# Kernel tuning notes

Hardware: AMD Instinct MI355X
Metric: run time of the kernel (lower is better)

## Reference

```python
import jax, jax.numpy as jnp
import numpy as np

BS, Z_DIM, HID, Z_IN, N_STEP, OUT_DIM = 4096, 512, 1024, 128, 32, 3


def setup_inputs() -> dict:
    key = jax.random.key(0)
    ks = jax.random.split(key, 12)
    s = 0.02
    return {
        "z": jax.random.normal(ks[0], (BS, Z_DIM), jnp.float32),
        "inference": 1,
        "tfr": 0,
        "W_zh": jax.random.normal(ks[1], (HID, Z_DIM), jnp.float32) * s,
        "b_zh": jnp.zeros((HID,), jnp.float32),
        "W_zi": jax.random.normal(ks[2], (Z_IN, Z_DIM), jnp.float32) * s,
        "b_zi": jnp.zeros((Z_IN,), jnp.float32),
        "W_ih": jax.random.normal(ks[3], (3 * HID, OUT_DIM + Z_IN), jnp.float32) * s,
        "b_ih": jnp.zeros((3 * HID,), jnp.float32),
        "W_hh": jax.random.normal(ks[4], (3 * HID, HID), jnp.float32) * s,
        "b_hh": jnp.zeros((3 * HID,), jnp.float32),
        "W_out": jax.random.normal(ks[5], (OUT_DIM, HID), jnp.float32) * s,
        "b_out": jnp.zeros((OUT_DIM,), jnp.float32),
        "init_input": jax.random.uniform(ks[6], (OUT_DIM,), jnp.float32),
    }


def reference(z, inference, tfr, W_zh, b_zh, W_zi, b_zi, W_ih, b_ih, W_hh, b_hh,
              W_out, b_out, init_input):
    bs = z.shape[0]
    h0 = z @ W_zh.T + b_zh                      # [B, H]   (z2dec_hid)
    z_in = z @ W_zi.T + b_zi                    # [B, Z_IN] (z2dec_in)
    token0 = jnp.broadcast_to(init_input, (bs, OUT_DIM))

    def step(carry, _):
        h, token = carry
        x = jnp.concatenate([token, z_in], axis=-1)     # [B, OUT_DIM+Z_IN]
        gi = x @ W_ih.T + b_ih                          # [B, 3H]
        gh = h @ W_hh.T + b_hh                          # [B, 3H]
        i_r, i_u, i_n = jnp.split(gi, 3, axis=-1)       # pytorch gate order r,z,n
        h_r, h_u, h_n = jnp.split(gh, 3, axis=-1)
        r = jax.nn.sigmoid(i_r + h_r)
        u = jax.nn.sigmoid(i_u + h_u)
        n = jnp.tanh(i_n + r * h_n)
        h_new = (1.0 - u) * n + u * h
        o = h_new @ W_out.T + b_out                     # [B, 3]
        bass = jax.nn.sigmoid(o[:, 0])
        rhy_int = o[:, 1]
        rhy = jax.nn.sigmoid(o[:, 2])
        out_feat = jnp.stack([bass, rhy_int, rhy], axis=-1)          # [B, 3]
        next_token = jnp.stack(
            [bass, rhy_int, (rhy > 0.5).astype(z.dtype)], axis=-1)  # [B, 3]
        return (h_new, next_token), out_feat

    _, outs = jax.lax.scan(step, (h0, token0), None, length=N_STEP)  # [T, B, 3]
    recon = jnp.transpose(outs, (1, 0, 2))                           # [B, T, 3]
    return recon
```

## Files before the change

kernel.cpp:

```cpp
#include <hip/hip_runtime.h>
#include <hip/hip_bf16.h>
#include <math.h>

#define BS   4096
#define ZD   512
#define HIDN 1024
#define ZINN 128
#define NST  32
#define NP   3072

typedef unsigned short u16;
typedef __bf16 bf16x8 __attribute__((ext_vector_type(8)));
typedef _Float16 f16x8 __attribute__((ext_vector_type(8)));
typedef float f32x4 __attribute__((ext_vector_type(4)));
typedef float f32x16 __attribute__((ext_vector_type(16)));

static __device__ __forceinline__ u16 bf_bits(float v) {
  __bf16 b = (__bf16)v;
  return __builtin_bit_cast(unsigned short, b);
}
static __device__ __forceinline__ float bf_val(float v) {
  return (float)(__bf16)v;
}
static __device__ __forceinline__ u16 h16_bits(float v) {
  _Float16 h = (_Float16)v;
  return __builtin_bit_cast(unsigned short, h);
}

static __device__ __forceinline__ void ld_lds16(const u16* g, u16* l) {
  __builtin_amdgcn_global_load_lds(
      (const __attribute__((address_space(1))) void*)g,
      (__attribute__((address_space(3))) void*)l, 16, 0, 0);
}

static __device__ __forceinline__ int r_orig(int w) {
  const int g = w / 96;
  const int rem = w - g * 96;
  const int j = rem >> 5, m = rem & 31;
  return j * 1024 + g * 32 + m;
}

static __device__ __forceinline__ size_t pk_off(int row, int col) {
  return ((size_t)(row >> 5) * 64 + (col >> 4)) * 512 +
         (((col >> 3) & 1) * 32 + (row & 31)) * 8 + (col & 7);
}
static __device__ __forceinline__ size_t pkz_off(int row, int col) {
  return ((size_t)(row >> 5) * 8 + (col >> 4)) * 512 +
         (((col >> 3) & 1) * 32 + (row & 31)) * 8 + (col & 7);
}


__global__ void k_split(const float* __restrict__ s, u16* __restrict__ hi,
                        u16* __restrict__ lo, int n) {
  int i = blockIdx.x * 256 + threadIdx.x;
  if (i >= n) return;
  float v = s[i];
  float h = bf_val(v);
  hi[i] = bf_bits(v);
  lo[i] = bf_bits(v - h);
}

__global__ void k_pack_whh(const float* __restrict__ W_hh, u16* __restrict__ Bpk) {
  int i = blockIdx.x * 256 + threadIdx.x;
  if (i >= NP * HIDN) return;
  const int w = i >> 10, k = i & 1023;
  const float v = W_hh[(size_t)r_orig(w) * HIDN + k];
  Bpk[pk_off(w, k)] = h16_bits(v);
}

__global__ void k_prep_wih(const float* __restrict__ W_ih, const float* __restrict__ b_ih,
                           const float* __restrict__ b_hh,
                           u16* __restrict__ Wpk,
                           float* __restrict__ wtok, float* __restrict__ cb0) {
  int i = blockIdx.x * 256 + threadIdx.x;
  if (i < NP * 128) {
    const int w = i >> 7, c = i & 127;
    const float v = W_ih[r_orig(w) * 131 + 3 + c];
    Wpk[pkz_off(w, c)] = h16_bits(v);
  }
  if (i < NP * 3) {
    const int w = i / 3, s = i - w * 3;
    wtok[i] = W_ih[r_orig(w) * 131 + s];
  }
  if (i < NP) {
    const int r = r_orig(i);
    cb0[i] = b_ih[r] + (r < 2048 ? b_hh[r] : 0.0f);
  }
}

__global__ void k_token_init(const float* __restrict__ init_input, float* __restrict__ token) {
  int i = blockIdx.x * 256 + threadIdx.x;
  if (i < BS * 4) token[i] = ((i & 3) < 3) ? init_input[i & 3] : 0.0f;
}

template <int OUTMODE>
__global__ __launch_bounds__(256) void k_gemm(
    const u16* __restrict__ Ahi, const u16* __restrict__ Alo,
    const u16* __restrict__ Bhi, const u16* __restrict__ Blo,
    const float* __restrict__ bias,
    float* __restrict__ C, u16* __restrict__ Apk, int N, int K) {
  __shared__ __align__(16) u16 sAhi[128 * 64];
  __shared__ __align__(16) u16 sAlo[128 * 64];
  __shared__ __align__(16) u16 sBhi[128 * 64];
  __shared__ __align__(16) u16 sBlo[128 * 64];

  const int t = threadIdx.x;
  const int row0 = blockIdx.y * 128, col0 = blockIdx.x * 128;
  const int wave = t >> 6, lane = t & 63;
  const int w64 = wave * 64;
  const int wm = (wave & 1) * 64, wn = (wave >> 1) * 64;
  const int lm = lane & 15, lq = lane >> 4;
  const int pb = lm & 7;

  f32x4 acc[4][4] = {};

  int sm[4], skc[4], sub[4];
#pragma unroll
  for (int i = 0; i < 4; ++i) {
    const int u = i * 256 + t;
    sm[i] = u >> 3;
    skc[i] = (u & 7) ^ (sm[i] & 7);
    sub[i] = (i * 256 + w64) * 8;
  }

  const int nk = K >> 6;
  for (int kt = 0; kt < nk; ++kt) {
    const int k0 = kt << 6;
    __syncthreads();
#pragma unroll
    for (int i = 0; i < 4; ++i) {
      const size_t ga = (size_t)(row0 + sm[i]) * K + k0 + skc[i] * 8;
      const size_t gb = (size_t)(col0 + sm[i]) * K + k0 + skc[i] * 8;
      ld_lds16(Ahi + ga, &sAhi[sub[i]]);
      ld_lds16(Alo + ga, &sAlo[sub[i]]);
      ld_lds16(Bhi + gb, &sBhi[sub[i]]);
      ld_lds16(Blo + gb, &sBlo[sub[i]]);
    }
    __syncthreads();
#pragma unroll
    for (int kk = 0; kk < 2; ++kk) {
      const int pos = ((kk * 4 + lq) ^ pb) * 8;
      bf16x8 ah[4], al[4], bh[4], bl[4];
#pragma unroll
      for (int i = 0; i < 4; ++i) {
        const int ma = (wm + i * 16 + lm) * 64;
        const int mb = (wn + i * 16 + lm) * 64;
        ah[i] = *(const bf16x8*)&sAhi[ma + pos];
        al[i] = *(const bf16x8*)&sAlo[ma + pos];
        bh[i] = *(const bf16x8*)&sBhi[mb + pos];
        bl[i] = *(const bf16x8*)&sBlo[mb + pos];
      }
#pragma unroll
      for (int i = 0; i < 4; ++i)
#pragma unroll
        for (int j = 0; j < 4; ++j) {
          acc[i][j] = __builtin_amdgcn_mfma_f32_16x16x32_bf16(ah[i], bh[j], acc[i][j], 0, 0, 0);
          acc[i][j] = __builtin_amdgcn_mfma_f32_16x16x32_bf16(al[i], bh[j], acc[i][j], 0, 0, 0);
          acc[i][j] = __builtin_amdgcn_mfma_f32_16x16x32_bf16(ah[i], bl[j], acc[i][j], 0, 0, 0);
        }
    }
  }

#pragma unroll
  for (int i = 0; i < 4; ++i) {
    const int grow = row0 + wm + i * 16 + lq * 4;
#pragma unroll
    for (int j = 0; j < 4; ++j) {
      const int gcol = col0 + wn + j * 16 + lm;
      const float bs = bias ? bias[gcol] : 0.0f;
#pragma unroll
      for (int d = 0; d < 4; ++d) {
        const float v = acc[i][j][d] + bs;
        if (OUTMODE == 2) {
          C[(size_t)(grow + d) * N + gcol] = v;
          Apk[pk_off(grow + d, gcol)] = h16_bits(v);
        }
        if (OUTMODE == 3) {
          Apk[pkz_off(grow + d, gcol)] = h16_bits(v);
        }
      }
    }
  }
}


#define SZA8 (128 * 64)
#define SZB8 (192 * 64)
#define MF8(a, b, c) c = __builtin_amdgcn_mfma_f32_32x32x16_f16(a, b, c, 0, 0, 0)

__global__ __launch_bounds__(512, 4) void k_fused10(
    const u16* __restrict__ Apk,
    const u16* __restrict__ Bpk,
    const u16* __restrict__ Zpk,
    const u16* __restrict__ Wpk,
    const float* __restrict__ token,
    const float* __restrict__ wtok,
    const float* __restrict__ cb0,
    const float* __restrict__ b_hh,
    const float* __restrict__ h_in, float* __restrict__ h_out,
    u16* __restrict__ Apk_out) {
  __shared__ __align__(16) u16 sA[2 * SZA8];
  __shared__ __align__(16) u16 sB[2 * SZB8];

  const int t = threadIdx.x;
  const int wave = t >> 6, lane = t & 63;
  const int row0 = blockIdx.y * 128;
  const int colW0 = blockIdx.x * 192;
  const int wm = (wave >> 1) * 32;
  const int wn = (wave & 1) * 96;
  const int lr = lane & 31, lh = lane >> 5;

  f32x16 acc0 = {}, acc1 = {}, acc2 = {}, acc3 = {};

  const u16* asrc = Apk + ((size_t)((row0 >> 5) + (wave >> 1)) * 64 + (wave & 1) * 2) * 512 + lane * 8;
  const int aw = (wave >> 1) * 2048 + (wave & 1) * 1024;
  const int id0 = wave * 3, id1 = id0 + 1, id2 = id0 + 2;
  const u16* bsrc0 = Bpk + ((size_t)((colW0 >> 5) + (id0 >> 2)) * 64 + (id0 & 3)) * 512 + lane * 8;
  const u16* bsrc1 = Bpk + ((size_t)((colW0 >> 5) + (id1 >> 2)) * 64 + (id1 & 3)) * 512 + lane * 8;
  const u16* bsrc2 = Bpk + ((size_t)((colW0 >> 5) + (id2 >> 2)) * 64 + (id2 & 3)) * 512 + lane * 8;
  const int bw0 = id0 * 512, bw1 = id1 * 512, bw2 = id2 * 512;
  const u16* azb = Zpk + ((size_t)((row0 >> 5) + (wave >> 1)) * 8 + (wave & 1) * 2) * 512 + lane * 8;
  const u16* bzb0 = Wpk + ((size_t)((colW0 >> 5) + (id0 >> 2)) * 8 + (id0 & 3)) * 512 + lane * 8;
  const u16* bzb1 = Wpk + ((size_t)((colW0 >> 5) + (id1 >> 2)) * 8 + (id1 & 3)) * 512 + lane * 8;
  const u16* bzb2 = Wpk + ((size_t)((colW0 >> 5) + (id2 >> 2)) * 8 + (id2 & 3)) * 512 + lane * 8;

#define STAGE(kt_, ab, bb)                                            \
  ld_lds16(asrc + (size_t)(kt_) * 2048,       &sA[(ab) + aw]);        \
  ld_lds16(asrc + (size_t)(kt_) * 2048 + 512, &sA[(ab) + aw + 512]);  \
  ld_lds16(bsrc0 + (size_t)(kt_) * 2048, &sB[(bb) + bw0]);            \
  ld_lds16(bsrc1 + (size_t)(kt_) * 2048, &sB[(bb) + bw1]);            \
  ld_lds16(bsrc2 + (size_t)(kt_) * 2048, &sB[(bb) + bw2]);

#define STAGE_Z(zt_, ab, bb)                                          \
  ld_lds16(azb + (zt_) * 2048,       &sA[(ab) + aw]);                 \
  ld_lds16(azb + (zt_) * 2048 + 512, &sA[(ab) + aw + 512]);           \
  ld_lds16(bzb0 + (zt_) * 2048, &sB[(bb) + bw0]);                     \
  ld_lds16(bzb1 + (zt_) * 2048, &sB[(bb) + bw1]);                     \
  ld_lds16(bzb2 + (zt_) * 2048, &sB[(bb) + bw2]);

  const int agA = (wave >> 1) * 2048;
  const int bgB = (wave & 1) * 6144;
  const int l8 = lane * 8;

  STAGE(0, 0, 0);
  __syncthreads();

#pragma unroll 1
  for (int kt = 0; kt < 16; ++kt) {
    const int ab = (kt & 1) ? SZA8 : 0, bb = (kt & 1) ? SZB8 : 0;
    const int an = (kt & 1) ? 0 : SZA8, bn = (kt & 1) ? 0 : SZB8;
    if (kt < 15) { STAGE(kt + 1, an, bn); }
    else         { STAGE_Z(0, an, bn); }
#pragma unroll
    for (int kk = 0; kk < 4; ++kk) {
      const f16x8 a = *(const f16x8*)&sA[ab + agA + kk * 512 + l8];
      const int kb = bb + bgB + kk * 512 + l8;
      const f16x8 b0 = *(const f16x8*)&sB[kb];
      const f16x8 b1 = *(const f16x8*)&sB[kb + 2048];
      const f16x8 b2 = *(const f16x8*)&sB[kb + 4096];
      MF8(a, b0, acc0); MF8(a, b1, acc1); MF8(a, b2, acc2);
    }
    __syncthreads();
  }
  STAGE_Z(1, SZA8, SZB8);
#pragma unroll
  for (int kk = 0; kk < 4; ++kk) {
    const f16x8 a = *(const f16x8*)&sA[agA + kk * 512 + l8];
    const int kb = bgB + kk * 512 + l8;
    const f16x8 b0 = *(const f16x8*)&sB[kb];
    const f16x8 b1 = *(const f16x8*)&sB[kb + 2048];
    const f16x8 b2 = *(const f16x8*)&sB[kb + 4096];
    MF8(a, b0, acc0); MF8(a, b1, acc1); MF8(a, b2, acc3);
  }
  __syncthreads();
#pragma unroll
  for (int kk = 0; kk < 4; ++kk) {
    const f16x8 a = *(const f16x8*)&sA[SZA8 + agA + kk * 512 + l8];
    const int kb = SZB8 + bgB + kk * 512 + l8;
    const f16x8 b0 = *(const f16x8*)&sB[kb];
    const f16x8 b1 = *(const f16x8*)&sB[kb + 2048];
    const f16x8 b2 = *(const f16x8*)&sB[kb + 4096];
    MF8(a, b0, acc0); MF8(a, b1, acc1); MF8(a, b2, acc3);
  }
#undef STAGE
#undef STAGE_Z

  const int w0 = colW0 + wn + lr;
  const int c = ((colW0 + wn) / 96) * 32 + lr;
  float wt[3][3];
#pragma unroll
  for (int j = 0; j < 3; ++j) {
    wt[j][0] = wtok[(w0 + j * 32) * 3 + 0];
    wt[j][1] = wtok[(w0 + j * 32) * 3 + 1];
    wt[j][2] = wtok[(w0 + j * 32) * 3 + 2];
  }
  const float cbr = cb0[w0], cbu = cb0[w0 + 32], cbn = cb0[w0 + 64];
  const float bnn = b_hh[2048 + c];
  const int cq = c >> 4, ckh = (c >> 3) & 1, ce = c & 7;
#pragma unroll
  for (int d = 0; d < 16; ++d) {
    const int row = row0 + wm + 4 * lh + (d & 3) + 8 * (d >> 2);
    const float4 tk = *(const float4*)&token[row * 4];
    const float pr = cbr + acc0[d] + tk.x * wt[0][0] + tk.y * wt[0][1] + tk.z * wt[0][2];
    const float pu = cbu + acc1[d] + tk.x * wt[1][0] + tk.y * wt[1][1] + tk.z * wt[1][2];
    const float pin = cbn + acc3[d] + tk.x * wt[2][0] + tk.y * wt[2][1] + tk.z * wt[2][2];
    const float hn = acc2[d] + bnn;
    const float r = 1.0f / (1.0f + expf(-pr));
    const float u = 1.0f / (1.0f + expf(-pu));
    const float n = tanhf(pin + r * hn);
    const size_t hidx = (size_t)row * HIDN + c;
    const float hv = (1.0f - u) * n + u * h_in[hidx];
    h_out[hidx] = hv;
    const size_t poff = ((size_t)(row >> 5) * 64 + cq) * 512 + (ckh * 32 + (row & 31)) * 8 + ce;
    Apk_out[poff] = h16_bits(hv);
  }
}
#undef MF8

__global__ __launch_bounds__(256) void k_out(
    const float* __restrict__ h, const float* __restrict__ W_out,
    const float* __restrict__ b_out,
    float* __restrict__ out, float* __restrict__ token, int step) {
  const int wave = threadIdx.x >> 6, lane = threadIdx.x & 63;
  const int row = blockIdx.x * 4 + wave;
  const float4* hp = (const float4*)(h + (size_t)row * 1024);
  const float4* w0p = (const float4*)(W_out);
  const float4* w1p = (const float4*)(W_out + 1024);
  const float4* w2p = (const float4*)(W_out + 2048);
  float s0 = 0.f, s1 = 0.f, s2 = 0.f;
#pragma unroll
  for (int c = 0; c < 4; ++c) {
    const int k = lane + 64 * c;
    const float4 hv = hp[k];
    const float4 a = w0p[k], bq = w1p[k], cq = w2p[k];
    s0 += hv.x * a.x + hv.y * a.y + hv.z * a.z + hv.w * a.w;
    s1 += hv.x * bq.x + hv.y * bq.y + hv.z * bq.z + hv.w * bq.w;
    s2 += hv.x * cq.x + hv.y * cq.y + hv.z * cq.z + hv.w * cq.w;
  }
#pragma unroll
  for (int off = 32; off > 0; off >>= 1) {
    s0 += __shfl_xor(s0, off, 64);
    s1 += __shfl_xor(s1, off, 64);
    s2 += __shfl_xor(s2, off, 64);
  }
  if (lane == 0) {
    const float o0 = s0 + b_out[0];
    const float o1 = s1 + b_out[1];
    const float o2 = s2 + b_out[2];
    const float bass = 1.0f / (1.0f + expf(-o0));
    const float rhy = 1.0f / (1.0f + expf(-o2));
    const size_t ob = ((size_t)row * NST + step) * 3;
    out[ob + 0] = bass;
    out[ob + 1] = o1;
    out[ob + 2] = rhy;
    token[row * 4 + 0] = bass;
    token[row * 4 + 1] = o1;
    token[row * 4 + 2] = (rhy > 0.5f) ? 1.0f : 0.0f;
  }
}

extern "C" void kernel_launch(void* const* d_in, const int* in_sizes, int n_in,
                              void* d_out, int out_size, void* d_ws, size_t ws_size,
                              hipStream_t stream) {
  const float* z = (const float*)d_in[0];
  const float* W_zh = (const float*)d_in[3];
  const float* b_zh = (const float*)d_in[4];
  const float* W_zi = (const float*)d_in[5];
  const float* b_zi = (const float*)d_in[6];
  const float* W_ih = (const float*)d_in[7];
  const float* b_ih = (const float*)d_in[8];
  const float* W_hh = (const float*)d_in[9];
  const float* b_hh = (const float*)d_in[10];
  const float* W_out = (const float*)d_in[11];
  const float* b_out = (const float*)d_in[12];
  const float* init_input = (const float*)d_in[13];
  float* out = (float*)d_out;

  char* p = (char*)d_ws;
  auto alloc = [&](size_t bytes) {
    char* q = p;
    p += (bytes + 255) & ~(size_t)255;
    return q;
  };
  float* h[2];
  u16* Apk[2];
  for (int s = 0; s < 2; ++s) {
    h[s] = (float*)alloc((size_t)BS * HIDN * 4);
    Apk[s] = (u16*)alloc((size_t)BS * 1024 * 2);
  }
  u16* Bpk = (u16*)alloc((size_t)NP * 1024 * 2);
  u16* Zpk = (u16*)alloc((size_t)BS * 128 * 2);
  u16* Wpk = (u16*)alloc((size_t)NP * 128 * 2);
  u16* z_hi = (u16*)alloc((size_t)BS * ZD * 2);
  u16* z_lo = (u16*)alloc((size_t)BS * ZD * 2);
  u16* Wzh_hi = (u16*)alloc((size_t)HIDN * ZD * 2);
  u16* Wzh_lo = (u16*)alloc((size_t)HIDN * ZD * 2);
  u16* Wzi_hi = (u16*)alloc((size_t)ZINN * ZD * 2);
  u16* Wzi_lo = (u16*)alloc((size_t)ZINN * ZD * 2);
  float* wtok = (float*)alloc((size_t)NP * 3 * 4);
  float* cb0 = (float*)alloc((size_t)NP * 4);
  float* token = (float*)alloc((size_t)BS * 4 * 4);

  k_pack_whh<<<dim3((NP * HIDN + 255) / 256), 256, 0, stream>>>(W_hh, Bpk);
  k_split<<<dim3((HIDN * ZD + 255) / 256), 256, 0, stream>>>(W_zh, Wzh_hi, Wzh_lo, HIDN * ZD);
  k_split<<<dim3((ZINN * ZD + 255) / 256), 256, 0, stream>>>(W_zi, Wzi_hi, Wzi_lo, ZINN * ZD);
  k_split<<<dim3((BS * ZD + 255) / 256), 256, 0, stream>>>(z, z_hi, z_lo, BS * ZD);
  k_prep_wih<<<dim3((NP * 128 + 255) / 256), 256, 0, stream>>>(W_ih, b_ih, b_hh, Wpk, wtok, cb0);
  k_token_init<<<dim3((BS * 4 + 255) / 256), 256, 0, stream>>>(init_input, token);

  k_gemm<2><<<dim3(HIDN / 128, BS / 128), 256, 0, stream>>>(
      z_hi, z_lo, Wzh_hi, Wzh_lo, b_zh, h[0], Apk[0], HIDN, ZD);
  k_gemm<3><<<dim3(ZINN / 128, BS / 128), 256, 0, stream>>>(
      z_hi, z_lo, Wzi_hi, Wzi_lo, b_zi, nullptr, Zpk, ZINN, ZD);

  for (int t = 0; t < NST; ++t) {
    const int cur = t & 1, nxt = (t + 1) & 1;
    k_fused10<<<dim3(NP / 192, BS / 128), 512, 0, stream>>>(
        Apk[cur], Bpk, Zpk, Wpk, token, wtok, cb0, b_hh,
        h[cur], h[nxt], Apk[nxt]);
    k_out<<<dim3(BS / 4), 256, 0, stream>>>(h[nxt], W_out, b_out, out, token, t);
  }
  (void)in_sizes; (void)n_in; (void)out_size; (void)ws_size;
}
```

Baseline: 1.710 ms.

## Triple-buffer fused GRU GEMM with smaller K tiles and read fp16 h in output kernel

The fused GRU step kernel moves from a double-buffered K=64 tile loop to a triple-buffered K=32 loop that prefetches two stages ahead. It uses explicit vmcnt waits and raw barriers in place of __syncthreads, so global-to-LDS loads overlap with MFMA work. The output projection kernel now reads the packed fp16 hidden state instead of the fp32 copy, which halves the bytes it reads. This adds fp16 rounding to the output logits, which could flip the thresholded rhythm token, and the hand-tuned waitcnt counts depend on exact load counts per wave.

Result: slower. 1.843 ms (+7.8%).

```diff
diff --git a/kernel.cpp b/kernel.cpp
--- a/kernel.cpp
+++ b/kernel.cpp
@@ -184,11 +184,11 @@
 }
 
 
-#define SZA8 (128 * 64)
-#define SZB8 (192 * 64)
-#define MF8(a, b, c) c = __builtin_amdgcn_mfma_f32_32x32x16_f16(a, b, c, 0, 0, 0)
-
-__global__ __launch_bounds__(512, 4) void k_fused10(
+#define SZA11 4096
+#define SZB11 6144
+#define MF11(a, b, c) c = __builtin_amdgcn_mfma_f32_32x32x16_f16(a, b, c, 0, 0, 0)
+
+__global__ __launch_bounds__(512, 4) void k_fused11(
     const u16* __restrict__ Apk,
     const u16* __restrict__ Bpk,
     const u16* __restrict__ Zpk,
@@ -199,8 +199,8 @@
     const float* __restrict__ b_hh,
     const float* __restrict__ h_in, float* __restrict__ h_out,
     u16* __restrict__ Apk_out) {
-  __shared__ __align__(16) u16 sA[2 * SZA8];
-  __shared__ __align__(16) u16 sB[2 * SZB8];
+  __shared__ __align__(16) u16 sA[3 * SZA11];
+  __shared__ __align__(16) u16 sB[3 * SZB11];
 
   const int t = threadIdx.x;
   const int wave = t >> 6, lane = t & 63;
@@ -209,80 +209,73 @@
   const int wm = (wave >> 1) * 32;
   const int wn = (wave & 1) * 96;
   const int lr = lane & 31, lh = lane >> 5;
+  const int l8 = lane * 8;
 
   f32x16 acc0 = {}, acc1 = {}, acc2 = {}, acc3 = {};
 
-  const u16* asrc = Apk + ((size_t)((row0 >> 5) + (wave >> 1)) * 64 + (wave & 1) * 2) * 512 + lane * 8;
-  const int aw = (wave >> 1) * 2048 + (wave & 1) * 1024;
-  const int id0 = wave * 3, id1 = id0 + 1, id2 = id0 + 2;
-  const u16* bsrc0 = Bpk + ((size_t)((colW0 >> 5) + (id0 >> 2)) * 64 + (id0 & 3)) * 512 + lane * 8;
-  const u16* bsrc1 = Bpk + ((size_t)((colW0 >> 5) + (id1 >> 2)) * 64 + (id1 & 3)) * 512 + lane * 8;
-  const u16* bsrc2 = Bpk + ((size_t)((colW0 >> 5) + (id2 >> 2)) * 64 + (id2 & 3)) * 512 + lane * 8;
-  const int bw0 = id0 * 512, bw1 = id1 * 512, bw2 = id2 * 512;
-  const u16* azb = Zpk + ((size_t)((row0 >> 5) + (wave >> 1)) * 8 + (wave & 1) * 2) * 512 + lane * 8;
-  const u16* bzb0 = Wpk + ((size_t)((colW0 >> 5) + (id0 >> 2)) * 8 + (id0 & 3)) * 512 + lane * 8;
-  const u16* bzb1 = Wpk + ((size_t)((colW0 >> 5) + (id1 >> 2)) * 8 + (id1 & 3)) * 512 + lane * 8;
-  const u16* bzb2 = Wpk + ((size_t)((colW0 >> 5) + (id2 >> 2)) * 8 + (id2 & 3)) * 512 + lane * 8;
-
-#define STAGE(kt_, ab, bb)                                            \
-  ld_lds16(asrc + (size_t)(kt_) * 2048,       &sA[(ab) + aw]);        \
-  ld_lds16(asrc + (size_t)(kt_) * 2048 + 512, &sA[(ab) + aw + 512]);  \
-  ld_lds16(bsrc0 + (size_t)(kt_) * 2048, &sB[(bb) + bw0]);            \
-  ld_lds16(bsrc1 + (size_t)(kt_) * 2048, &sB[(bb) + bw1]);            \
-  ld_lds16(bsrc2 + (size_t)(kt_) * 2048, &sB[(bb) + bw2]);
-
-#define STAGE_Z(zt_, ab, bb)                                          \
-  ld_lds16(azb + (zt_) * 2048,       &sA[(ab) + aw]);                 \
-  ld_lds16(azb + (zt_) * 2048 + 512, &sA[(ab) + aw + 512]);           \
-  ld_lds16(bzb0 + (zt_) * 2048, &sB[(bb) + bw0]);                     \
-  ld_lds16(bzb1 + (zt_) * 2048, &sB[(bb) + bw1]);                     \
-  ld_lds16(bzb2 + (zt_) * 2048, &sB[(bb) + bw2]);
-
-  const int agA = (wave >> 1) * 2048;
-  const int bgB = (wave & 1) * 6144;
-  const int l8 = lane * 8;
-
-  STAGE(0, 0, 0);
-  __syncthreads();
+  const bool twoB = (wave < 4);
+  const u16* aH = Apk + ((size_t)((row0 >> 5) + (wave >> 1)) * 64 + (wave & 1)) * 512 + l8;
+  const u16* aZ = Zpk + ((size_t)((row0 >> 5) + (wave >> 1)) * 8 + (wave & 1)) * 512 + l8;
+  const int awS = (wave >> 1) * 1024 + (wave & 1) * 512;
+  const int idA = wave;
+  const int idB = twoB ? (8 + wave) : 0;
+  const u16* bH0 = Bpk + ((size_t)((colW0 >> 5) + (idA >> 1)) * 64 + (idA & 1)) * 512 + l8;
+  const u16* bH1 = Bpk + ((size_t)((colW0 >> 5) + (idB >> 1)) * 64 + (idB & 1)) * 512 + l8;
+  const u16* bZ0 = Wpk + ((size_t)((colW0 >> 5) + (idA >> 1)) * 8 + (idA & 1)) * 512 + l8;
+  const u16* bZ1 = Wpk + ((size_t)((colW0 >> 5) + (idB >> 1)) * 8 + (idB & 1)) * 512 + l8;
+  const int bwS0 = idA * 512, bwS1 = idB * 512;
+
+#define STAGE_H(kt_, ab, bb)                                     \
+  ld_lds16(aH + (size_t)(kt_) * 1024, &sA[(ab) + awS]);          \
+  ld_lds16(bH0 + (size_t)(kt_) * 1024, &sB[(bb) + bwS0]);        \
+  if (twoB) { ld_lds16(bH1 + (size_t)(kt_) * 1024, &sB[(bb) + bwS1]); }
+
+#define STAGE_Z(zt_, ab, bb)                                     \
+  ld_lds16(aZ + (zt_) * 1024, &sA[(ab) + awS]);                  \
+  ld_lds16(bZ0 + (zt_) * 1024, &sB[(bb) + bwS0]);                \
+  if (twoB) { ld_lds16(bZ1 + (zt_) * 1024, &sB[(bb) + bwS1]); }
+
+  const int agA = (wave >> 1) * 1024;
+  const int bgB = (wave & 1) * 3072;
+
+  STAGE_H(0, 0, 0);
+  STAGE_H(1, SZA11, SZB11);
+  if (twoB) { asm volatile("s_waitcnt vmcnt(3)" ::: "memory"); }
+  else      { asm volatile("s_waitcnt vmcnt(2)" ::: "memory"); }
+  __builtin_amdgcn_s_barrier();
+
+  int oA0 = 0, oA1 = SZA11, oA2 = 2 * SZA11;
+  int oB0 = 0, oB1 = SZB11, oB2 = 2 * SZB11;
 
 #pragma unroll 1
-  for (int kt = 0; kt < 16; ++kt) {
-    const int ab = (kt & 1) ? SZA8 : 0, bb = (kt & 1) ? SZB8 : 0;
-    const int an = (kt & 1) ? 0 : SZA8, bn = (kt & 1) ? 0 : SZB8;
-    if (kt < 15) { STAGE(kt + 1, an, bn); }
-    else         { STAGE_Z(0, an, bn); }
-#pragma unroll
-    for (int kk = 0; kk < 4; ++kk) {
-      const f16x8 a = *(const f16x8*)&sA[ab + agA + kk * 512 + l8];
-      const int kb = bb + bgB + kk * 512 + l8;
+  for (int kt = 0; kt < 36; ++kt) {
+    const int nt = kt + 2;
+    if (nt < 32)      { STAGE_H(nt, oA2, oB2); }
+    else if (nt < 36) { STAGE_Z(nt - 32, oA2, oB2); }
+#pragma unroll
+    for (int kk = 0; kk < 2; ++kk) {
+      const f16x8 a = *(const f16x8*)&sA[oA0 + agA + kk * 512 + l8];
+      const int kb = oB0 + bgB + kk * 512 + l8;
       const f16x8 b0 = *(const f16x8*)&sB[kb];
-      const f16x8 b1 = *(const f16x8*)&sB[kb + 2048];
-      const f16x8 b2 = *(const f16x8*)&sB[kb + 4096];
-      MF8(a, b0, acc0); MF8(a, b1, acc1); MF8(a, b2, acc2);
-    }
-    __syncthreads();
-  }
-  STAGE_Z(1, SZA8, SZB8);
-#pragma unroll
-  for (int kk = 0; kk < 4; ++kk) {
-    const f16x8 a = *(const f16x8*)&sA[agA + kk * 512 + l8];
-    const int kb = bgB + kk * 512 + l8;
-    const f16x8 b0 = *(const f16x8*)&sB[kb];
-    const f16x8 b1 = *(const f16x8*)&sB[kb + 2048];
-    const f16x8 b2 = *(const f16x8*)&sB[kb + 4096];
-    MF8(a, b0, acc0); MF8(a, b1, acc1); MF8(a, b2, acc3);
-  }
-  __syncthreads();
-#pragma unroll
-  for (int kk = 0; kk < 4; ++kk) {
-    const f16x8 a = *(const f16x8*)&sA[SZA8 + agA + kk * 512 + l8];
-    const int kb = SZB8 + bgB + kk * 512 + l8;
-    const f16x8 b0 = *(const f16x8*)&sB[kb];
-    const f16x8 b1 = *(const f16x8*)&sB[kb + 2048];
-    const f16x8 b2 = *(const f16x8*)&sB[kb + 4096];
-    MF8(a, b0, acc0); MF8(a, b1, acc1); MF8(a, b2, acc3);
-  }
-#undef STAGE
+      const f16x8 b1 = *(const f16x8*)&sB[kb + 1024];
+      const f16x8 b2 = *(const f16x8*)&sB[kb + 2048];
+      MF11(a, b0, acc0);
+      MF11(a, b1, acc1);
+      if (kt < 32) { MF11(a, b2, acc2); }
+      else         { MF11(a, b2, acc3); }
+    }
+    if (kt < 34) {
+      if (twoB) { asm volatile("s_waitcnt vmcnt(3)" ::: "memory"); }
+      else      { asm volatile("s_waitcnt vmcnt(2)" ::: "memory"); }
+      __builtin_amdgcn_s_barrier();
+    } else if (kt == 34) {
+      asm volatile("s_waitcnt vmcnt(0)" ::: "memory");
+      __builtin_amdgcn_s_barrier();
+    }
+    const int tA = oA0; oA0 = oA1; oA1 = oA2; oA2 = tA;
+    const int tB = oB0; oB0 = oB1; oB1 = oB2; oB2 = tB;
+  }
+#undef STAGE_H
 #undef STAGE_Z
 
   const int w0 = colW0 + wn + lr;
@@ -315,27 +308,28 @@
     Apk_out[poff] = h16_bits(hv);
   }
 }
-#undef MF8
+#undef MF11
 
 __global__ __launch_bounds__(256) void k_out(
-    const float* __restrict__ h, const float* __restrict__ W_out,
+    const u16* __restrict__ Apk, const float* __restrict__ W_out,
     const float* __restrict__ b_out,
     float* __restrict__ out, float* __restrict__ token, int step) {
   const int wave = threadIdx.x >> 6, lane = threadIdx.x & 63;
   const int row = blockIdx.x * 4 + wave;
-  const float4* hp = (const float4*)(h + (size_t)row * 1024);
-  const float4* w0p = (const float4*)(W_out);
-  const float4* w1p = (const float4*)(W_out + 1024);
-  const float4* w2p = (const float4*)(W_out + 2048);
+  const u16* base = Apk + (size_t)(row >> 5) * 64 * 512 + (row & 31) * 8;
   float s0 = 0.f, s1 = 0.f, s2 = 0.f;
 #pragma unroll
-  for (int c = 0; c < 4; ++c) {
-    const int k = lane + 64 * c;
-    const float4 hv = hp[k];
-    const float4 a = w0p[k], bq = w1p[k], cq = w2p[k];
-    s0 += hv.x * a.x + hv.y * a.y + hv.z * a.z + hv.w * a.w;
-    s1 += hv.x * bq.x + hv.y * bq.y + hv.z * bq.z + hv.w * bq.w;
-    s2 += hv.x * cq.x + hv.y * cq.y + hv.z * cq.z + hv.w * cq.w;
+  for (int cc = 0; cc < 2; ++cc) {
+    const int ch = lane + cc * 64;
+    const f16x8 hv = *(const f16x8*)&base[(ch >> 1) * 512 + (ch & 1) * 256];
+    const int k0 = ch * 8;
+#pragma unroll
+    for (int e = 0; e < 8; ++e) {
+      const float hf = (float)hv[e];
+      s0 += hf * W_out[k0 + e];
+      s1 += hf * W_out[1024 + k0 + e];
+      s2 += hf * W_out[2048 + k0 + e];
+    }
   }
 #pragma unroll
   for (int off = 32; off > 0; off >>= 1) {
@@ -415,10 +409,10 @@
 
   for (int t = 0; t < NST; ++t) {
     const int cur = t & 1, nxt = (t + 1) & 1;
-    k_fused10<<<dim3(NP / 192, BS / 128), 512, 0, stream>>>(
+    k_fused11<<<dim3(NP / 192, BS / 128), 512, 0, stream>>>(
         Apk[cur], Bpk, Zpk, Wpk, token, wtok, cb0, b_hh,
         h[cur], h[nxt], Apk[nxt]);
-    k_out<<<dim3(BS / 4), 256, 0, stream>>>(h[nxt], W_out, b_out, out, token, t);
+    k_out<<<dim3(BS / 4), 256, 0, stream>>>(Apk[nxt], W_out, b_out, out, token, t);
   }
   (void)in_sizes; (void)n_in; (void)out_size; (void)ws_size;
 }
```
